# Kernel tuning notes

Measured on AMD Instinct MI355X. Metric: run time of the kernel, lower is better.

Reference implementation:

```python
import jax, jax.numpy as jnp
import numpy as np

N = 100000   # nodes
E = 1600000  # edges
D = 128      # in_channels
H = 128      # hidden_dim
L = 3        # num_layers
LH = 128     # lstm_hidden
OUT = 16     # output_dim
G = 128      # graphs in batch
EPS = 1e-5   # BatchNorm eps


def setup_inputs() -> dict:
    key = jax.random.key(0)
    ks = jax.random.split(key, 14)
    x = jax.random.normal(ks[0], (N, D), jnp.float32)
    src = jax.random.randint(ks[1], (E,), 0, N)
    dst = jax.random.randint(ks[2], (E,), 0, N)
    edge_index = jnp.stack([src, dst])
    batch = jnp.sort(jax.random.randint(ks[3], (N,), 0, G))
    Ws = jax.random.normal(ks[4], (L, D, H), jnp.float32) / np.float32(np.sqrt(D))
    bs = jax.random.normal(ks[5], (L, H), jnp.float32) * 0.02
    gammas = 1.0 + 0.1 * jax.random.normal(ks[6], (L, H), jnp.float32)
    betas = 0.1 * jax.random.normal(ks[7], (L, H), jnp.float32)
    rms = 0.1 * jax.random.normal(ks[8], (L, H), jnp.float32)
    rvs = jax.random.uniform(ks[9], (L, H), jnp.float32, 0.5, 1.5)
    W_ih = jax.random.normal(ks[10], (4 * LH, H), jnp.float32) / np.float32(np.sqrt(H))
    W_hh = jax.random.normal(ks[11], (4 * LH, LH), jnp.float32) / np.float32(np.sqrt(LH))
    b_ih = jnp.zeros((4 * LH,), jnp.float32)
    b_hh = jnp.zeros((4 * LH,), jnp.float32)
    W_fc = jax.random.normal(ks[12], (OUT, LH), jnp.float32) / np.float32(np.sqrt(LH))
    b_fc = 0.02 * jax.random.normal(ks[13], (OUT,), jnp.float32)
    return dict(x=x, edge_index=edge_index, batch=batch, Ws=Ws, bs=bs,
                gammas=gammas, betas=betas, rms=rms, rvs=rvs,
                W_ih=W_ih, W_hh=W_hh, b_ih=b_ih, b_hh=b_hh, W_fc=W_fc, b_fc=b_fc)


def reference(x, edge_index, batch, Ws, bs, gammas, betas, rms, rvs,
              W_ih, W_hh, b_ih, b_hh, W_fc, b_fc):
    # GCNConv: add self-loops, symmetric deg^-1/2 normalization
    src, dst = edge_index[0], edge_index[1]
    loop = jnp.arange(N)
    s = jnp.concatenate([src, loop])
    d = jnp.concatenate([dst, loop])
    deg = jax.ops.segment_sum(jnp.ones((E + N,), x.dtype), d, num_segments=N)
    dinv = jax.lax.rsqrt(jnp.maximum(deg, 1.0))  # deg >= 1 due to self-loops
    norm = (dinv[s] * dinv[d])[:, None]          # [E+N, 1]
    h = x
    for l in range(L):
        h = h @ Ws[l]                                                  # [N, H]
        agg = jax.ops.segment_sum(h[s] * norm, d, num_segments=N) + bs[l]
        # BatchNorm (eval: running stats) -> dropout (eval: identity) -> ReLU
        y = (agg - rms[l]) * (gammas[l] * jax.lax.rsqrt(rvs[l] + EPS)) + betas[l]
        h = jax.nn.relu(y)
    # global_mean_pool
    sums = jax.ops.segment_sum(h, batch, num_segments=G)               # [G, H]
    cnt = jax.ops.segment_sum(jnp.ones((N,), h.dtype), batch, num_segments=G)
    pooled = sums / jnp.maximum(cnt, 1.0)[:, None]
    # single-timestep LSTM, h0 = c0 = 0 -> forget gate contributes nothing
    gates = pooled @ W_ih.T + b_ih + b_hh                              # [G, 4*LH]
    i, f, g, o = jnp.split(gates, 4, axis=-1)
    c = jax.nn.sigmoid(i) * jnp.tanh(g)
    hn = jax.nn.sigmoid(o) * jnp.tanh(c)
    return hn @ W_fc.T + b_fc                                          # [G, OUT]
```

## Files before the change

kernel.cpp:

```cpp
#include <hip/hip_runtime.h>
#include <math.h>

constexpr int   NN  = 100000;
constexpr int   EE  = 1600000;
constexpr int   HH  = 128;
constexpr int   GG  = 128;
constexpr float EPSV = 1e-5f;
constexpr int   NSH = 8;
constexpr int   SHN = NN / NSH;
constexpr int   CAP = 210000;
constexpr int   NSB = 32;
constexpr int   SUBW = (SHN + NSB - 1) / NSB;
constexpr int   CAP2 = 8192;
constexpr int   NCH = 64;

typedef __attribute__((ext_vector_type(8))) short  short8;
typedef __attribute__((ext_vector_type(4))) float  f32x4;
typedef __attribute__((ext_vector_type(2))) float  v2f;

__device__ __forceinline__ unsigned short f2bf(float f) {
    union { float f; unsigned u; } v; v.f = f;
    unsigned r = v.u + 0x7FFF + ((v.u >> 16) & 1);
    return (unsigned short)(r >> 16);
}
__device__ __forceinline__ float bf2f(unsigned short b) {
    union { unsigned u; float f; } v; v.u = ((unsigned)b) << 16;
    return v.f;
}

constexpr size_t A256(size_t x) { return (x + 255) & ~(size_t)255; }
constexpr size_t OFF_TL  = 0;
constexpr size_t OFF_DNV = A256(OFF_TL  + (8 + 256 + 256) * 4);
constexpr size_t OFF_RP  = A256(OFF_DNV + (size_t)NN * 4);
constexpr size_t OFF_SRC = A256(OFF_RP  + (size_t)(NN + 1) * 4);
constexpr size_t OFF_BIN = A256(OFF_SRC + (size_t)EE * 4);
constexpr size_t OFF_B2  = A256(OFF_BIN + (size_t)8 * CAP * 4);
constexpr size_t OFF_HW  = A256(OFF_B2  + (size_t)256 * CAP2 * 4);
constexpr size_t OFF_H0  = A256(OFF_HW  + (size_t)NN * HH * 2);
constexpr size_t OFF_PL  = A256(OFF_H0  + (size_t)NN * HH * 2);

__global__ __launch_bounds__(256) void k_bin(const int* __restrict__ src,
                                             const int* __restrict__ dst,
                                             unsigned* __restrict__ bins,
                                             unsigned* __restrict__ gtail) {
    __shared__ unsigned sbin[8][1024];
    __shared__ unsigned scnt[8];
    __shared__ unsigned sbase[8];
    int t = threadIdx.x;
    if (t < 8) scnt[t] = 0;
    __syncthreads();
    int i = blockIdx.x * 256 + t;
    const int nvec = EE / 4;
    if (i < nvec) {
        int4 d = ((const int4*)dst)[i];
        int4 s = ((const int4*)src)[i];
        int dd[4] = {d.x, d.y, d.z, d.w};
        int ss[4] = {s.x, s.y, s.z, s.w};
#pragma unroll
        for (int c = 0; c < 4; ++c) {
            int sh = dd[c] / SHN;
            unsigned p = atomicAdd(&scnt[sh], 1u);
            sbin[sh][p] = ((unsigned)(dd[c] - sh * SHN) << 17) | (unsigned)ss[c];
        }
    }
    __syncthreads();
    if (t < 8) sbase[t] = atomicAdd(&gtail[t], scnt[t]);
    __syncthreads();
    for (int s = 0; s < 8; ++s) {
        unsigned cnt = scnt[s], base = sbase[s];
        if (base >= (unsigned)CAP) continue;
        if (base + cnt > (unsigned)CAP) cnt = CAP - base;
        for (unsigned j = t; j < cnt; j += 256)
            bins[(size_t)s * CAP + base + j] = sbin[s][j];
    }
}

__global__ __launch_bounds__(256) void k_bin2(const unsigned* __restrict__ bins,
                                              const unsigned* __restrict__ gtail,
                                              unsigned* __restrict__ bins2,
                                              unsigned* __restrict__ tail2) {
    __shared__ unsigned staged[(CAP + NCH - 1) / NCH + 64];
    __shared__ unsigned cnt[NSB], base[NSB], cur[NSB], gbase[NSB];
    int t = threadIdx.x;
    int shard = blockIdx.x >> 6, chunk = blockIdx.x & 63;
    unsigned m = gtail[shard];
    if (m > (unsigned)CAP) m = CAP;
    unsigned csz = (m + NCH - 1) / NCH;
    unsigned i0 = chunk * csz;
    unsigned i1 = i0 + csz; if (i1 > m) i1 = m;
    if (i0 >= m) return;
    const unsigned* bb = bins + (size_t)shard * CAP;

    if (t < NSB) cnt[t] = 0;
    __syncthreads();
    for (unsigned i = i0 + t; i < i1; i += 256)
        atomicAdd(&cnt[(bb[i] >> 17) / SUBW], 1u);
    __syncthreads();
    if (t == 0) {
        unsigned run = 0;
        for (int sb = 0; sb < NSB; ++sb) { base[sb] = run; run += cnt[sb]; }
    }
    __syncthreads();
    if (t < NSB) {
        gbase[t] = atomicAdd(&tail2[shard * NSB + t], cnt[t]);
        cur[t] = base[t];
    }
    __syncthreads();
    for (unsigned i = i0 + t; i < i1; i += 256) {
        unsigned u = bb[i];
        unsigned dl = u >> 17;
        unsigned sb = dl / SUBW;
        unsigned p = atomicAdd(&cur[sb], 1u);
        staged[p] = ((dl - sb * SUBW) << 17) | (u & 0x1FFFFu);
    }
    __syncthreads();
    int wv = t >> 6, ln = t & 63;
    for (int sb = wv; sb < NSB; sb += 4) {
        unsigned c = cnt[sb], gb = gbase[sb], lb = base[sb];
        if (gb >= (unsigned)CAP2) continue;
        if (gb + c > (unsigned)CAP2) c = CAP2 - gb;
        unsigned* dstp = bins2 + (size_t)(shard * NSB + sb) * CAP2 + gb;
        for (unsigned j = ln; j < c; j += 64) dstp[j] = staged[lb + j];
    }
}

__global__ __launch_bounds__(256) void k_tailscan(const unsigned* __restrict__ tail2,
                                                  unsigned* __restrict__ sbase,
                                                  float* __restrict__ pooled) {
    __shared__ unsigned sa[256], sd[256];
    int t = threadIdx.x;
    unsigned v = tail2[t];
    sa[t] = v;
    __syncthreads();
    unsigned* s = sa; unsigned* d = sd;
    for (int off = 1; off < 256; off <<= 1) {
        d[t] = s[t] + ((t >= off) ? s[t - off] : 0u);
        __syncthreads();
        unsigned* tmp = s; s = d; d = tmp;
    }
    sbase[t] = s[t] - v;
    for (int i = t; i < GG * HH + GG; i += 256) pooled[i] = 0.f;
}

__global__ __launch_bounds__(256) void k_hist3(const unsigned* __restrict__ bins2,
                                               const unsigned* __restrict__ tail2,
                                               const unsigned* __restrict__ sbase,
                                               int* __restrict__ rp,
                                               float* __restrict__ dinv) {
    int b = blockIdx.x;
    int shard = b >> 5, sb = b & 31;
    int lo = sb * SUBW;
    int hi = lo + SUBW; if (hi > SHN) hi = SHN;
    int nn = hi - lo;
    int gbase = shard * SHN + lo;
    __shared__ int hist[SUBW];
    __shared__ int sa[512], sd[512];
    int t = threadIdx.x;
    for (int i = t; i < nn; i += 256) hist[i] = 0;
    __syncthreads();
    unsigned m = tail2[b];
    if (m > (unsigned)CAP2) m = CAP2;
    const unsigned* bb = bins2 + (size_t)b * CAP2;
    unsigned nv = m >> 2;
    for (unsigned i = t; i < nv; i += 256) {
        uint4 u = ((const uint4*)bb)[i];
        atomicAdd(&hist[u.x >> 17], 1);
        atomicAdd(&hist[u.y >> 17], 1);
        atomicAdd(&hist[u.z >> 17], 1);
        atomicAdd(&hist[u.w >> 17], 1);
    }
    for (unsigned i = (m & ~3u) + t; i < m; i += 256)
        atomicAdd(&hist[bb[i] >> 17], 1);
    __syncthreads();
    sa[t]       = (t < nn)       ? hist[t]       : 0;
    sa[t + 256] = (t + 256 < nn) ? hist[t + 256] : 0;
    __syncthreads();
    int* s = sa; int* d = sd;
    for (int off = 1; off < 512; off <<= 1) {
        d[t]       = s[t]       + ((t >= off)       ? s[t - off]       : 0);
        d[t + 256] = s[t + 256] + ((t + 256 >= off) ? s[t + 256 - off] : 0);
        __syncthreads();
        int* tmp = s; s = d; d = tmp;
    }
    unsigned base = sbase[b];
    for (int i = t; i < nn; i += 256) {
        rp[gbase + i]   = (int)(base + (i ? (unsigned)s[i - 1] : 0u));
        dinv[gbase + i] = rsqrtf((float)(hist[i] + 1));
    }
    if (b == 255 && t == 0) rp[NN] = EE;
}

__global__ __launch_bounds__(256) void k_scatter4(const unsigned* __restrict__ bins2,
                                                  const unsigned* __restrict__ tail2,
                                                  const int* __restrict__ rp,
                                                  int* __restrict__ ssrc) {
    int b = blockIdx.x;
    int shard = b >> 5, sb = b & 31;
    int lo = sb * SUBW;
    int hi = lo + SUBW; if (hi > SHN) hi = SHN;
    int nn = hi - lo;
    int gbase = shard * SHN + lo;
    __shared__ int cur[SUBW];
    int t = threadIdx.x;
    for (int i = t; i < nn; i += 256) cur[i] = rp[gbase + i];
    __syncthreads();
    unsigned m = tail2[b];
    if (m > (unsigned)CAP2) m = CAP2;
    const unsigned* bb = bins2 + (size_t)b * CAP2;
    unsigned nv = m >> 2;
    for (unsigned i = t; i < nv; i += 256) {
        uint4 u = ((const uint4*)bb)[i];
        int p;
        p = atomicAdd(&cur[u.x >> 17], 1); ssrc[p] = (int)(u.x & 0x1FFFFu);
        p = atomicAdd(&cur[u.y >> 17], 1); ssrc[p] = (int)(u.y & 0x1FFFFu);
        p = atomicAdd(&cur[u.z >> 17], 1); ssrc[p] = (int)(u.z & 0x1FFFFu);
        p = atomicAdd(&cur[u.w >> 17], 1); ssrc[p] = (int)(u.w & 0x1FFFFu);
    }
    for (unsigned i = (m & ~3u) + t; i < m; i += 256) {
        unsigned u = bb[i];
        int p = atomicAdd(&cur[u >> 17], 1);
        ssrc[p] = (int)(u & 0x1FFFFu);
    }
}

template<bool FP32A>
__global__ __launch_bounds__(256) void gemm_mfma(const void* __restrict__ Ap,
                                                 const float* __restrict__ W,
                                                 unsigned short* __restrict__ C, int nrows) {
    __shared__ unsigned short WtH[64 * 136];
    __shared__ unsigned short WtL[64 * 136];
    int t = threadIdx.x;
    int row0 = blockIdx.x * 128;
    int wv = t >> 6, lane = t & 63, m = lane & 15, q = lane >> 4;
    long rowA = row0 + wv * 32 + m;
    long rowB = rowA + 16;

    short8 a[2][4];
#pragma unroll
    for (int kc = 0; kc < 4; ++kc) {
        int ko = kc * 32 + q * 8;
        if (FP32A) {
            const float* Af = (const float*)Ap;
            float4 f0 = {0,0,0,0}, f1 = {0,0,0,0}, g0 = {0,0,0,0}, g1 = {0,0,0,0};
            if (rowA < nrows) {
                f0 = *(const float4*)(Af + rowA * 128 + ko);
                f1 = *(const float4*)(Af + rowA * 128 + ko + 4);
            }
            if (rowB < nrows) {
                g0 = *(const float4*)(Af + rowB * 128 + ko);
                g1 = *(const float4*)(Af + rowB * 128 + ko + 4);
            }
            union { short8 s; unsigned short u[8]; } ua, ub;
            ua.u[0] = f2bf(f0.x); ua.u[1] = f2bf(f0.y); ua.u[2] = f2bf(f0.z); ua.u[3] = f2bf(f0.w);
            ua.u[4] = f2bf(f1.x); ua.u[5] = f2bf(f1.y); ua.u[6] = f2bf(f1.z); ua.u[7] = f2bf(f1.w);
            ub.u[0] = f2bf(g0.x); ub.u[1] = f2bf(g0.y); ub.u[2] = f2bf(g0.z); ub.u[3] = f2bf(g0.w);
            ub.u[4] = f2bf(g1.x); ub.u[5] = f2bf(g1.y); ub.u[6] = f2bf(g1.z); ub.u[7] = f2bf(g1.w);
            a[0][kc] = ua.s; a[1][kc] = ub.s;
        } else {
            const unsigned short* Ab = (const unsigned short*)Ap;
            short8 z = {};
            a[0][kc] = (rowA < nrows) ? *(const short8*)(Ab + rowA * 128 + ko) : z;
            a[1][kc] = (rowB < nrows) ? *(const short8*)(Ab + rowB * 128 + ko) : z;
        }
    }

    for (int half = 0; half < 2; ++half) {
        int c0 = half * 64;
        __syncthreads();
        for (int idx = t; idx < 64 * 128; idx += 256) {
            int k = idx >> 6, c = idx & 63;
            float w = W[k * 128 + c0 + c];
            unsigned short hb = f2bf(w);
            WtH[c * 136 + k] = hb;
            WtL[c * 136 + k] = f2bf(w - bf2f(hb));
        }
        __syncthreads();
        f32x4 acc[2][4] = {};
#pragma unroll
        for (int kc = 0; kc < 4; ++kc) {
            int ko = kc * 32 + q * 8;
#pragma unroll
            for (int ct = 0; ct < 4; ++ct) {
                short8 bh = *(const short8*)(WtH + (ct * 16 + m) * 136 + ko);
                short8 bl = *(const short8*)(WtL + (ct * 16 + m) * 136 + ko);
                acc[0][ct] = __builtin_amdgcn_mfma_f32_16x16x32_bf16(a[0][kc], bh, acc[0][ct], 0, 0, 0);
                acc[0][ct] = __builtin_amdgcn_mfma_f32_16x16x32_bf16(a[0][kc], bl, acc[0][ct], 0, 0, 0);
                acc[1][ct] = __builtin_amdgcn_mfma_f32_16x16x32_bf16(a[1][kc], bh, acc[1][ct], 0, 0, 0);
                acc[1][ct] = __builtin_amdgcn_mfma_f32_16x16x32_bf16(a[1][kc], bl, acc[1][ct], 0, 0, 0);
            }
        }
        __syncthreads();
        unsigned short* Cs = WtH;
#pragma unroll
        for (int rt = 0; rt < 2; ++rt)
#pragma unroll
            for (int ct = 0; ct < 4; ++ct)
#pragma unroll
                for (int r = 0; r < 4; ++r) {
                    int rl = wv * 32 + rt * 16 + q * 4 + r;
                    Cs[rl * 68 + ct * 16 + m] = f2bf(acc[rt][ct][r]);
                }
        __syncthreads();
        for (int idx = t; idx < 128 * 16; idx += 256) {
            int row = idx >> 4, ch = idx & 15;
            long grow = row0 + row;
            if (grow < nrows)
                *(ushort4*)(C + grow * 128 + c0 + ch * 4) = *(const ushort4*)(Cs + row * 68 + ch * 4);
        }
    }
}

__global__ __launch_bounds__(256) void k_agg(const unsigned short* __restrict__ hw,
                                             const int* __restrict__ rp,
                                             const int* __restrict__ ssrc,
                                             const float* __restrict__ dinv,
                                             const float* __restrict__ bsl,
                                             const float* __restrict__ gamma,
                                             const float* __restrict__ beta,
                                             const float* __restrict__ rm,
                                             const float* __restrict__ rv,
                                             unsigned short* __restrict__ out) {
    int lane = threadIdx.x & 63;
    int c2   = lane * 2;
    int n = blockIdx.x * 4 + (threadIdx.x >> 6);
    if (n >= NN) return;
    int beg = rp[n], end = rp[n + 1];

    v2f acc0 = {0.f, 0.f}, acc1 = {0.f, 0.f};

    for (int chunk = beg; chunk < end; chunk += 64) {
        int l = chunk + lane;
        bool valid = (l < end);
        int   e  = valid ? ssrc[l] : n;
        float dv = valid ? dinv[e] : 0.f;
        int cnt = end - chunk;
        if (cnt > 64) cnt = 64;
        for (int jb = 0; jb < cnt; jb += 8) {
#pragma unroll
            for (int j = 0; j < 8; ++j) {
                int s    = __builtin_amdgcn_readlane(e, jb + j);
                float ds = __int_as_float(
                               __builtin_amdgcn_readlane(__float_as_int(dv), jb + j));
                unsigned u = *(const unsigned*)(hw + (size_t)s * HH + c2);
                v2f vv;
                vv.x = __int_as_float((int)(u << 16));
                vv.y = __int_as_float((int)(u & 0xffff0000u));
                v2f d2 = {ds, ds};
                if (j & 1) acc1 += d2 * vv;
                else       acc0 += d2 * vv;
            }
        }
    }
    v2f a = acc0 + acc1;

    float di = dinv[n];
    {
        unsigned u = *(const unsigned*)(hw + (size_t)n * HH + c2);
        v2f vv;
        vv.x = __int_as_float((int)(u << 16));
        vv.y = __int_as_float((int)(u & 0xffff0000u));
        v2f d2 = {di, di};
        a += d2 * vv;
    }
    a.x *= di;
    a.y *= di;

    float g0 = gamma[c2],   g1 = gamma[c2 + 1];
    float r0 = rv[c2],      r1 = rv[c2 + 1];
    float s0 = g0 * rsqrtf(r0 + EPSV);
    float s1 = g1 * rsqrtf(r1 + EPSV);
    float b0 = fmaf(bsl[c2]     - rm[c2],     s0, beta[c2]);
    float b1 = fmaf(bsl[c2 + 1] - rm[c2 + 1], s1, beta[c2 + 1]);
    float y0 = fmaxf(fmaf(a.x, s0, b0), 0.f);
    float y1 = fmaxf(fmaf(a.y, s1, b1), 0.f);
    ushort2 o;
    o.x = f2bf(y0);
    o.y = f2bf(y1);
    *(ushort2*)(out + (size_t)n * HH + c2) = o;
}

__global__ __launch_bounds__(128) void k_pool(const unsigned short* __restrict__ h,
                                              const int* __restrict__ batch,
                                              float* __restrict__ pooled,
                                              float* __restrict__ cnt) {
    int t = threadIdx.x;
    const int chunk = (NN + 1023) / 1024;
    int n0 = blockIdx.x * chunk;
    if (n0 >= NN) return;
    int n1 = n0 + chunk;
    if (n1 > NN) n1 = NN;
    int cur = batch[n0];
    float acc = 0.f;
    int k = 0;
    for (int n = n0; n < n1; ++n) {
        int b = batch[n];
        if (b != cur) {
            atomicAdd(&pooled[(size_t)cur * 128 + t], acc);
            if (t == 0) atomicAdd(&cnt[cur], (float)k);
            acc = 0.f; k = 0; cur = b;
        }
        acc += bf2f(h[(size_t)n * 128 + t]);
        ++k;
    }
    atomicAdd(&pooled[(size_t)cur * 128 + t], acc);
    if (t == 0) atomicAdd(&cnt[cur], (float)k);
}

__global__ __launch_bounds__(128) void k_head(const float* __restrict__ pooled,
                                              const float* __restrict__ cnt,
                                              const float* __restrict__ W_ih,
                                              const float* __restrict__ b_ih,
                                              const float* __restrict__ b_hh,
                                              const float* __restrict__ W_fc,
                                              const float* __restrict__ b_fc,
                                              float* __restrict__ out) {
    __shared__ float pm[128];
    __shared__ float gate[512];
    __shared__ float hn[128];
    int g = blockIdx.x, t = threadIdx.x;
    float cdiv = fmaxf(cnt[g], 1.0f);
    pm[t] = pooled[(size_t)g * 128 + t] / cdiv;
    __syncthreads();
    for (int j = t; j < 512; j += 128) {
        float acc = b_ih[j] + b_hh[j];
        const float* w = W_ih + (size_t)j * 128;
#pragma unroll 8
        for (int k = 0; k < 128; ++k) acc = fmaf(pm[k], w[k], acc);
        gate[j] = acc;
    }
    __syncthreads();
    {
        float gi = gate[t], gg = gate[256 + t], go = gate[384 + t];
        float cc = (1.f / (1.f + expf(-gi))) * tanhf(gg);
        hn[t] = (1.f / (1.f + expf(-go))) * tanhf(cc);
    }
    __syncthreads();
    if (t < 16) {
        float acc = b_fc[t];
        const float* w = W_fc + (size_t)t * 128;
#pragma unroll 8
        for (int k = 0; k < 128; ++k) acc = fmaf(hn[k], w[k], acc);
        out[(size_t)g * 16 + t] = acc;
    }
}

extern "C" void kernel_launch(void* const* d_in, const int* in_sizes, int n_in,
                              void* d_out, int out_size, void* d_ws, size_t ws_size,
                              hipStream_t stream) {
    const float* x      = (const float*)d_in[0];
    const int*   ei     = (const int*)d_in[1];
    const int*   src    = ei;
    const int*   dst    = ei + EE;
    const int*   batch  = (const int*)d_in[2];
    const float* Ws     = (const float*)d_in[3];
    const float* bs     = (const float*)d_in[4];
    const float* gammas = (const float*)d_in[5];
    const float* betas  = (const float*)d_in[6];
    const float* rms    = (const float*)d_in[7];
    const float* rvs    = (const float*)d_in[8];
    const float* W_ih   = (const float*)d_in[9];
    const float* b_ih   = (const float*)d_in[11];
    const float* b_hh   = (const float*)d_in[12];
    const float* W_fc   = (const float*)d_in[13];
    const float* b_fc   = (const float*)d_in[14];
    float* out = (float*)d_out;

    char* w = (char*)d_ws;
    unsigned*       gtail  = (unsigned*)(w + OFF_TL);
    unsigned*       tail2  = gtail + 8;
    unsigned*       sbase  = gtail + 8 + 256;
    float*          dinv   = (float*)(w + OFF_DNV);
    int*            rp     = (int*)(w + OFF_RP);
    int*            ssrc   = (int*)(w + OFF_SRC);
    unsigned*       bins   = (unsigned*)(w + OFF_BIN);
    unsigned*       bins2  = (unsigned*)(w + OFF_B2);
    unsigned short* hwb    = (unsigned short*)(w + OFF_HW);
    unsigned short* h0     = (unsigned short*)(w + OFF_H0);
    float*          pooled = (float*)(w + OFF_PL);
    float*          cntb   = pooled + (size_t)GG * HH;

    hipMemsetAsync(gtail, 0, (8 + 256) * 4, stream);

    k_bin<<<(EE / 4 + 255) / 256, 256, 0, stream>>>(src, dst, bins, gtail);
    k_bin2<<<NSH * NCH, 256, 0, stream>>>(bins, gtail, bins2, tail2);
    k_tailscan<<<1, 256, 0, stream>>>(tail2, sbase, pooled);
    k_hist3<<<256, 256, 0, stream>>>(bins2, tail2, sbase, rp, dinv);
    k_scatter4<<<256, 256, 0, stream>>>(bins2, tail2, rp, ssrc);

    dim3 ggrid((NN + 127) / 128);
    for (int l = 0; l < 3; ++l) {
        if (l == 0)
            gemm_mfma<true><<<ggrid, 256, 0, stream>>>(x, Ws, hwb, NN);
        else
            gemm_mfma<false><<<ggrid, 256, 0, stream>>>(h0, Ws + (size_t)l * 128 * 128, hwb, NN);
        k_agg<<<(NN + 3) / 4, 256, 0, stream>>>(hwb, rp, ssrc, dinv,
                                                bs + l * 128, gammas + l * 128, betas + l * 128,
                                                rms + l * 128, rvs + l * 128, h0);
    }
    k_pool<<<1024, 128, 0, stream>>>(h0, batch, pooled, cntb);
    k_head<<<GG, 128, 0, stream>>>(pooled, cntb, W_ih, b_ih, b_hh, W_fc, b_fc, out);
}
```

Baseline: 475.5 us.

## Fuse CSR build into single-pass binning overlapped with first GEMM

Replaces the two-level edge binning (8 shards, then 32 sub-bins each) with one binning pass straight into 256 destination buckets. That pass runs as extra blocks inside the first-layer GEMM launch, so graph preprocessing overlaps with the matmul. The tail scan, histogram and scatter are merged into one k_build kernel, cutting five launches and the intermediate bins buffer. In exchange, dst is read twice, there is more global atomic contention on 256 tails, and the GEMM and binning branches share one kernel's resource footprint (both shared-memory sets are allocated).

```diff
diff --git a/kernel.cpp b/kernel.cpp
--- a/kernel.cpp
+++ b/kernel.cpp
@@ -6,13 +6,10 @@
 constexpr int   HH  = 128;
 constexpr int   GG  = 128;
 constexpr float EPSV = 1e-5f;
-constexpr int   NSH = 8;
-constexpr int   SHN = NN / NSH;
-constexpr int   CAP = 210000;
-constexpr int   NSB = 32;
-constexpr int   SUBW = (SHN + NSB - 1) / NSB;
+constexpr int   NSB = 256;
+constexpr int   SUBW = (NN + NSB - 1) / NSB;
 constexpr int   CAP2 = 8192;
-constexpr int   NCH = 64;
+constexpr int   GEMM_BLOCKS = (NN + 127) / 128;
 
 typedef __attribute__((ext_vector_type(8))) short  short8;
 typedef __attribute__((ext_vector_type(4))) float  f32x4;
@@ -30,207 +27,23 @@
 
 constexpr size_t A256(size_t x) { return (x + 255) & ~(size_t)255; }
 constexpr size_t OFF_TL  = 0;
-constexpr size_t OFF_DNV = A256(OFF_TL  + (8 + 256 + 256) * 4);
+constexpr size_t OFF_DNV = A256(OFF_TL  + 256 * 4);
 constexpr size_t OFF_RP  = A256(OFF_DNV + (size_t)NN * 4);
 constexpr size_t OFF_SRC = A256(OFF_RP  + (size_t)(NN + 1) * 4);
-constexpr size_t OFF_BIN = A256(OFF_SRC + (size_t)EE * 4);
-constexpr size_t OFF_B2  = A256(OFF_BIN + (size_t)8 * CAP * 4);
-constexpr size_t OFF_HW  = A256(OFF_B2  + (size_t)256 * CAP2 * 4);
+constexpr size_t OFF_B2  = A256(OFF_SRC + (size_t)EE * 4);
+constexpr size_t OFF_HW  = A256(OFF_B2  + (size_t)NSB * CAP2 * 4);
 constexpr size_t OFF_H0  = A256(OFF_HW  + (size_t)NN * HH * 2);
 constexpr size_t OFF_PL  = A256(OFF_H0  + (size_t)NN * HH * 2);
 
-__global__ __launch_bounds__(256) void k_bin(const int* __restrict__ src,
-                                             const int* __restrict__ dst,
-                                             unsigned* __restrict__ bins,
-                                             unsigned* __restrict__ gtail) {
-    __shared__ unsigned sbin[8][1024];
-    __shared__ unsigned scnt[8];
-    __shared__ unsigned sbase[8];
-    int t = threadIdx.x;
-    if (t < 8) scnt[t] = 0;
-    __syncthreads();
-    int i = blockIdx.x * 256 + t;
-    const int nvec = EE / 4;
-    if (i < nvec) {
-        int4 d = ((const int4*)dst)[i];
-        int4 s = ((const int4*)src)[i];
-        int dd[4] = {d.x, d.y, d.z, d.w};
-        int ss[4] = {s.x, s.y, s.z, s.w};
-#pragma unroll
-        for (int c = 0; c < 4; ++c) {
-            int sh = dd[c] / SHN;
-            unsigned p = atomicAdd(&scnt[sh], 1u);
-            sbin[sh][p] = ((unsigned)(dd[c] - sh * SHN) << 17) | (unsigned)ss[c];
-        }
-    }
-    __syncthreads();
-    if (t < 8) sbase[t] = atomicAdd(&gtail[t], scnt[t]);
-    __syncthreads();
-    for (int s = 0; s < 8; ++s) {
-        unsigned cnt = scnt[s], base = sbase[s];
-        if (base >= (unsigned)CAP) continue;
-        if (base + cnt > (unsigned)CAP) cnt = CAP - base;
-        for (unsigned j = t; j < cnt; j += 256)
-            bins[(size_t)s * CAP + base + j] = sbin[s][j];
-    }
-}
-
-__global__ __launch_bounds__(256) void k_bin2(const unsigned* __restrict__ bins,
-                                              const unsigned* __restrict__ gtail,
-                                              unsigned* __restrict__ bins2,
-                                              unsigned* __restrict__ tail2) {
-    __shared__ unsigned staged[(CAP + NCH - 1) / NCH + 64];
-    __shared__ unsigned cnt[NSB], base[NSB], cur[NSB], gbase[NSB];
-    int t = threadIdx.x;
-    int shard = blockIdx.x >> 6, chunk = blockIdx.x & 63;
-    unsigned m = gtail[shard];
-    if (m > (unsigned)CAP) m = CAP;
-    unsigned csz = (m + NCH - 1) / NCH;
-    unsigned i0 = chunk * csz;
-    unsigned i1 = i0 + csz; if (i1 > m) i1 = m;
-    if (i0 >= m) return;
-    const unsigned* bb = bins + (size_t)shard * CAP;
-
-    if (t < NSB) cnt[t] = 0;
-    __syncthreads();
-    for (unsigned i = i0 + t; i < i1; i += 256)
-        atomicAdd(&cnt[(bb[i] >> 17) / SUBW], 1u);
-    __syncthreads();
-    if (t == 0) {
-        unsigned run = 0;
-        for (int sb = 0; sb < NSB; ++sb) { base[sb] = run; run += cnt[sb]; }
-    }
-    __syncthreads();
-    if (t < NSB) {
-        gbase[t] = atomicAdd(&tail2[shard * NSB + t], cnt[t]);
-        cur[t] = base[t];
-    }
-    __syncthreads();
-    for (unsigned i = i0 + t; i < i1; i += 256) {
-        unsigned u = bb[i];
-        unsigned dl = u >> 17;
-        unsigned sb = dl / SUBW;
-        unsigned p = atomicAdd(&cur[sb], 1u);
-        staged[p] = ((dl - sb * SUBW) << 17) | (u & 0x1FFFFu);
-    }
-    __syncthreads();
-    int wv = t >> 6, ln = t & 63;
-    for (int sb = wv; sb < NSB; sb += 4) {
-        unsigned c = cnt[sb], gb = gbase[sb], lb = base[sb];
-        if (gb >= (unsigned)CAP2) continue;
-        if (gb + c > (unsigned)CAP2) c = CAP2 - gb;
-        unsigned* dstp = bins2 + (size_t)(shard * NSB + sb) * CAP2 + gb;
-        for (unsigned j = ln; j < c; j += 64) dstp[j] = staged[lb + j];
-    }
-}
-
-__global__ __launch_bounds__(256) void k_tailscan(const unsigned* __restrict__ tail2,
-                                                  unsigned* __restrict__ sbase,
-                                                  float* __restrict__ pooled) {
-    __shared__ unsigned sa[256], sd[256];
-    int t = threadIdx.x;
-    unsigned v = tail2[t];
-    sa[t] = v;
-    __syncthreads();
-    unsigned* s = sa; unsigned* d = sd;
-    for (int off = 1; off < 256; off <<= 1) {
-        d[t] = s[t] + ((t >= off) ? s[t - off] : 0u);
-        __syncthreads();
-        unsigned* tmp = s; s = d; d = tmp;
-    }
-    sbase[t] = s[t] - v;
-    for (int i = t; i < GG * HH + GG; i += 256) pooled[i] = 0.f;
-}
-
-__global__ __launch_bounds__(256) void k_hist3(const unsigned* __restrict__ bins2,
-                                               const unsigned* __restrict__ tail2,
-                                               const unsigned* __restrict__ sbase,
-                                               int* __restrict__ rp,
-                                               float* __restrict__ dinv) {
-    int b = blockIdx.x;
-    int shard = b >> 5, sb = b & 31;
-    int lo = sb * SUBW;
-    int hi = lo + SUBW; if (hi > SHN) hi = SHN;
-    int nn = hi - lo;
-    int gbase = shard * SHN + lo;
-    __shared__ int hist[SUBW];
-    __shared__ int sa[512], sd[512];
-    int t = threadIdx.x;
-    for (int i = t; i < nn; i += 256) hist[i] = 0;
-    __syncthreads();
-    unsigned m = tail2[b];
-    if (m > (unsigned)CAP2) m = CAP2;
-    const unsigned* bb = bins2 + (size_t)b * CAP2;
-    unsigned nv = m >> 2;
-    for (unsigned i = t; i < nv; i += 256) {
-        uint4 u = ((const uint4*)bb)[i];
-        atomicAdd(&hist[u.x >> 17], 1);
-        atomicAdd(&hist[u.y >> 17], 1);
-        atomicAdd(&hist[u.z >> 17], 1);
-        atomicAdd(&hist[u.w >> 17], 1);
-    }
-    for (unsigned i = (m & ~3u) + t; i < m; i += 256)
-        atomicAdd(&hist[bb[i] >> 17], 1);
-    __syncthreads();
-    sa[t]       = (t < nn)       ? hist[t]       : 0;
-    sa[t + 256] = (t + 256 < nn) ? hist[t + 256] : 0;
-    __syncthreads();
-    int* s = sa; int* d = sd;
-    for (int off = 1; off < 512; off <<= 1) {
-        d[t]       = s[t]       + ((t >= off)       ? s[t - off]       : 0);
-        d[t + 256] = s[t + 256] + ((t + 256 >= off) ? s[t + 256 - off] : 0);
-        __syncthreads();
-        int* tmp = s; s = d; d = tmp;
-    }
-    unsigned base = sbase[b];
-    for (int i = t; i < nn; i += 256) {
-        rp[gbase + i]   = (int)(base + (i ? (unsigned)s[i - 1] : 0u));
-        dinv[gbase + i] = rsqrtf((float)(hist[i] + 1));
-    }
-    if (b == 255 && t == 0) rp[NN] = EE;
-}
-
-__global__ __launch_bounds__(256) void k_scatter4(const unsigned* __restrict__ bins2,
-                                                  const unsigned* __restrict__ tail2,
-                                                  const int* __restrict__ rp,
-                                                  int* __restrict__ ssrc) {
-    int b = blockIdx.x;
-    int shard = b >> 5, sb = b & 31;
-    int lo = sb * SUBW;
-    int hi = lo + SUBW; if (hi > SHN) hi = SHN;
-    int nn = hi - lo;
-    int gbase = shard * SHN + lo;
-    __shared__ int cur[SUBW];
-    int t = threadIdx.x;
-    for (int i = t; i < nn; i += 256) cur[i] = rp[gbase + i];
-    __syncthreads();
-    unsigned m = tail2[b];
-    if (m > (unsigned)CAP2) m = CAP2;
-    const unsigned* bb = bins2 + (size_t)b * CAP2;
-    unsigned nv = m >> 2;
-    for (unsigned i = t; i < nv; i += 256) {
-        uint4 u = ((const uint4*)bb)[i];
-        int p;
-        p = atomicAdd(&cur[u.x >> 17], 1); ssrc[p] = (int)(u.x & 0x1FFFFu);
-        p = atomicAdd(&cur[u.y >> 17], 1); ssrc[p] = (int)(u.y & 0x1FFFFu);
-        p = atomicAdd(&cur[u.z >> 17], 1); ssrc[p] = (int)(u.z & 0x1FFFFu);
-        p = atomicAdd(&cur[u.w >> 17], 1); ssrc[p] = (int)(u.w & 0x1FFFFu);
-    }
-    for (unsigned i = (m & ~3u) + t; i < m; i += 256) {
-        unsigned u = bb[i];
-        int p = atomicAdd(&cur[u >> 17], 1);
-        ssrc[p] = (int)(u & 0x1FFFFu);
-    }
-}
-
 template<bool FP32A>
-__global__ __launch_bounds__(256) void gemm_mfma(const void* __restrict__ Ap,
-                                                 const float* __restrict__ W,
-                                                 unsigned short* __restrict__ C, int nrows) {
+__device__ __forceinline__ void gemm_body(const void* __restrict__ Ap,
+                                          const float* __restrict__ W,
+                                          unsigned short* __restrict__ C,
+                                          int nrows, int rb) {
     __shared__ unsigned short WtH[64 * 136];
     __shared__ unsigned short WtL[64 * 136];
     int t = threadIdx.x;
-    int row0 = blockIdx.x * 128;
+    int row0 = rb * 128;
     int wv = t >> 6, lane = t & 63, m = lane & 15, q = lane >> 4;
     long rowA = row0 + wv * 32 + m;
     long rowB = rowA + 16;
@@ -310,6 +123,149 @@
     }
 }
 
+__device__ void binall_body(const int* __restrict__ src, const int* __restrict__ dst,
+                            unsigned* __restrict__ bins2, unsigned* __restrict__ tail2,
+                            int b) {
+    __shared__ unsigned cnt[NSB];
+    __shared__ unsigned cur[NSB];
+    int t = threadIdx.x;
+    cnt[t] = 0;
+    __syncthreads();
+    const int nvec = EE / 4;
+    int csz = (nvec + NSB - 1) / NSB;
+    int i0 = b * csz;
+    int i1 = i0 + csz; if (i1 > nvec) i1 = nvec;
+    const int4* d4 = (const int4*)dst;
+    const int4* s4 = (const int4*)src;
+    for (int i = i0 + t; i < i1; i += 256) {
+        int4 d = d4[i];
+        atomicAdd(&cnt[(unsigned)d.x / SUBW], 1u);
+        atomicAdd(&cnt[(unsigned)d.y / SUBW], 1u);
+        atomicAdd(&cnt[(unsigned)d.z / SUBW], 1u);
+        atomicAdd(&cnt[(unsigned)d.w / SUBW], 1u);
+    }
+    __syncthreads();
+    cur[t] = atomicAdd(&tail2[t], cnt[t]);
+    __syncthreads();
+    for (int i = i0 + t; i < i1; i += 256) {
+        int4 d = d4[i];
+        int4 s = s4[i];
+        int dd[4] = {d.x, d.y, d.z, d.w};
+        int ss[4] = {s.x, s.y, s.z, s.w};
+#pragma unroll
+        for (int c = 0; c < 4; ++c) {
+            unsigned gsb = (unsigned)dd[c] / SUBW;
+            unsigned p = atomicAdd(&cur[gsb], 1u);
+            if (p < (unsigned)CAP2)
+                bins2[(size_t)gsb * CAP2 + p] =
+                    ((unsigned)(dd[c] - gsb * SUBW) << 17) | (unsigned)ss[c];
+        }
+    }
+}
+
+__global__ __launch_bounds__(256) void k_gemm0_bin(const float* __restrict__ x,
+                                                   const float* __restrict__ W,
+                                                   unsigned short* __restrict__ C,
+                                                   const int* __restrict__ src,
+                                                   const int* __restrict__ dst,
+                                                   unsigned* __restrict__ bins2,
+                                                   unsigned* __restrict__ tail2) {
+    if (blockIdx.x < GEMM_BLOCKS)
+        gemm_body<true>(x, W, C, NN, blockIdx.x);
+    else
+        binall_body(src, dst, bins2, tail2, blockIdx.x - GEMM_BLOCKS);
+}
+
+__global__ __launch_bounds__(256) void k_gemm(const unsigned short* __restrict__ A,
+                                              const float* __restrict__ W,
+                                              unsigned short* __restrict__ C) {
+    gemm_body<false>(A, W, C, NN, blockIdx.x);
+}
+
+__global__ __launch_bounds__(256) void k_build(const unsigned* __restrict__ bins2,
+                                               const unsigned* __restrict__ tail2,
+                                               int* __restrict__ rp,
+                                               float* __restrict__ dinv,
+                                               int* __restrict__ ssrc,
+                                               float* __restrict__ pooled) {
+    __shared__ int hist[SUBW];
+    __shared__ int sa[512], sd[512];
+    __shared__ unsigned ta[256], tb[256];
+    int b = blockIdx.x, t = threadIdx.x;
+
+    if (b < 65) {
+        int idx = b * 256 + t;
+        if (idx < GG * HH + GG) pooled[idx] = 0.f;
+    }
+
+    unsigned v = tail2[t];
+    ta[t] = v;
+    __syncthreads();
+    unsigned *sp = ta, *dp = tb;
+    for (int off = 1; off < 256; off <<= 1) {
+        dp[t] = sp[t] + ((t >= off) ? sp[t - off] : 0u);
+        __syncthreads();
+        unsigned* tmp = sp; sp = dp; dp = tmp;
+    }
+    unsigned base = sp[b] - tail2[b];
+    unsigned m = tail2[b];
+    if (m > (unsigned)CAP2) m = CAP2;
+
+    int lo = b * SUBW;
+    int nn = NN - lo; if (nn > SUBW) nn = SUBW;
+    for (int i = t; i < nn; i += 256) hist[i] = 0;
+    __syncthreads();
+
+    const unsigned* bb = bins2 + (size_t)b * CAP2;
+    unsigned nv = m >> 2;
+    for (unsigned i = t; i < nv; i += 256) {
+        uint4 u = ((const uint4*)bb)[i];
+        atomicAdd(&hist[u.x >> 17], 1);
+        atomicAdd(&hist[u.y >> 17], 1);
+        atomicAdd(&hist[u.z >> 17], 1);
+        atomicAdd(&hist[u.w >> 17], 1);
+    }
+    for (unsigned i = (m & ~3u) + t; i < m; i += 256)
+        atomicAdd(&hist[bb[i] >> 17], 1);
+    __syncthreads();
+
+    sa[t]       = (t < nn)       ? hist[t]       : 0;
+    sa[t + 256] = (t + 256 < nn) ? hist[t + 256] : 0;
+    __syncthreads();
+    int* s = sa; int* d = sd;
+    for (int off = 1; off < 512; off <<= 1) {
+        d[t]       = s[t]       + ((t >= off)       ? s[t - off]       : 0);
+        d[t + 256] = s[t + 256] + ((t + 256 >= off) ? s[t + 256 - off] : 0);
+        __syncthreads();
+        int* tmp = s; s = d; d = tmp;
+    }
+
+    for (int i = t; i < nn; i += 256) {
+        int cur0 = (int)base + (i ? s[i - 1] : 0);
+        rp[lo + i]   = cur0;
+        dinv[lo + i] = rsqrtf((float)(hist[i] + 1));
+    }
+    __syncthreads();
+    for (int i = t; i < nn; i += 256)
+        hist[i] = (int)base + (i ? s[i - 1] : 0);
+    if (b == 255 && t == 0) rp[NN] = EE;
+    __syncthreads();
+
+    for (unsigned i = t; i < nv; i += 256) {
+        uint4 u = ((const uint4*)bb)[i];
+        int p;
+        p = atomicAdd(&hist[u.x >> 17], 1); ssrc[p] = (int)(u.x & 0x1FFFFu);
+        p = atomicAdd(&hist[u.y >> 17], 1); ssrc[p] = (int)(u.y & 0x1FFFFu);
+        p = atomicAdd(&hist[u.z >> 17], 1); ssrc[p] = (int)(u.z & 0x1FFFFu);
+        p = atomicAdd(&hist[u.w >> 17], 1); ssrc[p] = (int)(u.w & 0x1FFFFu);
+    }
+    for (unsigned i = (m & ~3u) + t; i < m; i += 256) {
+        unsigned u = bb[i];
+        int p = atomicAdd(&hist[u >> 17], 1);
+        ssrc[p] = (int)(u & 0x1FFFFu);
+    }
+}
+
 __global__ __launch_bounds__(256) void k_agg(const unsigned short* __restrict__ hw,
                                              const int* __restrict__ rp,
                                              const int* __restrict__ ssrc,
@@ -466,33 +422,24 @@
     float* out = (float*)d_out;
 
     char* w = (char*)d_ws;
-    unsigned*       gtail  = (unsigned*)(w + OFF_TL);
-    unsigned*       tail2  = gtail + 8;
-    unsigned*       sbase  = gtail + 8 + 256;
+    unsigned*       tail2  = (unsigned*)(w + OFF_TL);
     float*          dinv   = (float*)(w + OFF_DNV);
     int*            rp     = (int*)(w + OFF_RP);
     int*            ssrc   = (int*)(w + OFF_SRC);
-    unsigned*       bins   = (unsigned*)(w + OFF_BIN);
     unsigned*       bins2  = (unsigned*)(w + OFF_B2);
     unsigned short* hwb    = (unsigned short*)(w + OFF_HW);
     unsigned short* h0     = (unsigned short*)(w + OFF_H0);
     float*          pooled = (float*)(w + OFF_PL);
     float*          cntb   = pooled + (size_t)GG * HH;
 
-    hipMemsetAsync(gtail, 0, (8 + 256) * 4, stream);
-
-    k_bin<<<(EE / 4 + 255) / 256, 256, 0, stream>>>(src, dst, bins, gtail);
-    k_bin2<<<NSH * NCH, 256, 0, stream>>>(bins, gtail, bins2, tail2);
-    k_tailscan<<<1, 256, 0, stream>>>(tail2, sbase, pooled);
-    k_hist3<<<256, 256, 0, stream>>>(bins2, tail2, sbase, rp, dinv);
-    k_scatter4<<<256, 256, 0, stream>>>(bins2, tail2, rp, ssrc);
-
-    dim3 ggrid((NN + 127) / 128);
+    hipMemsetAsync(tail2, 0, 256 * 4, stream);
+
+    k_gemm0_bin<<<GEMM_BLOCKS + NSB, 256, 0, stream>>>(x, Ws, hwb, src, dst, bins2, tail2);
+    k_build<<<NSB, 256, 0, stream>>>(bins2, tail2, rp, dinv, ssrc, pooled);
+
     for (int l = 0; l < 3; ++l) {
-        if (l == 0)
-            gemm_mfma<true><<<ggrid, 256, 0, stream>>>(x, Ws, hwb, NN);
-        else
-            gemm_mfma<false><<<ggrid, 256, 0, stream>>>(h0, Ws + (size_t)l * 128 * 128, hwb, NN);
+        if (l > 0)
+            k_gemm<<<GEMM_BLOCKS, 256, 0, stream>>>(h0, Ws + (size_t)l * 128 * 128, hwb);
         k_agg<<<(NN + 3) / 4, 256, 0, stream>>>(hwb, rp, ssrc, dinv,
                                                 bs + l * 128, gammas + l * 128, betas + l * 128,
                                                 rms + l * 128, rvs + l * 128, h0);
```

After: 443.2 us. -6.8%, faster.
